# Optimization experiments

Measured on AMD Instinct MI355X. Metric: run time of the kernel, lower is better.

The kernel has to match this reference:

```python
import jax, jax.numpy as jnp
import numpy as np

B, V_IN, V_OUT, C_IN, C_OUT, K, NNZ = 16, 1024, 4096, 128, 256, 18, 16384

def setup_inputs() -> dict:
    key = jax.random.key(0)
    ks = jax.random.split(key, 10)
    def lin(k, fan_in, fan_out):
        s = 1.0 / np.sqrt(fan_in)
        return jax.random.normal(k, (fan_in, fan_out), jnp.float32) * s
    return {
        "x": jax.random.normal(ks[0], (B, V_IN, C_IN), jnp.float32),
        "vals": jax.random.uniform(ks[1], (NNZ,), jnp.float32),
        "W1": lin(ks[2], 1 * C_IN, C_OUT),
        "b1": jnp.zeros((C_OUT,), jnp.float32),
        "Wd3": lin(ks[3], (K // 3) * C_IN, C_OUT // 4),
        "bd3": jnp.zeros((C_OUT // 4,), jnp.float32),
        "W2d3": lin(ks[4], (K // 3 * 2) * C_IN, C_OUT // 4),
        "b2d3": jnp.zeros((C_OUT // 4,), jnp.float32),
        "Wf": lin(ks[5], K * C_IN, C_OUT // 2),
        "bf": jnp.zeros((C_OUT // 2,), jnp.float32),
        "rows": jax.random.randint(ks[6], (NNZ,), 0, V_OUT, jnp.int32),
        "cols": jax.random.randint(ks[7], (NNZ,), 0, V_IN, jnp.int32),
        "spiral_idx": jax.random.randint(ks[8], (V_OUT, K), 0, V_OUT, jnp.int32),
    }

def _pool(x, rows, cols, vals, dim_size):
    # sparse upsample: gather cols, scale, scatter-add to rows
    gathered = x[:, cols, :] * vals[None, :, None]  # [B, nnz, C]
    return jnp.zeros((x.shape[0], dim_size, x.shape[2]), x.dtype).at[:, rows, :].add(gathered)

def _spiral_conv(feat, idx, W, b):
    # gather fixed spiral neighborhoods then shared linear layer
    Bz, V, C = feat.shape[0], idx.shape[0], feat.shape[2]
    g = feat[:, idx.reshape(-1), :].reshape(Bz, V, idx.shape[1] * C)  # [B, V, K*C]
    return g @ W + b

def reference(x, vals, W1, b1, Wd3, bd3, W2d3, b2d3, Wf, bf, rows, cols, spiral_idx):
    out = _pool(x, rows, cols, vals, V_OUT)  # [B, V_OUT, C_IN]
    k = spiral_idx.shape[1]
    short_cut = _spiral_conv(out, spiral_idx[:, :1], W1, b1)
    p_d3 = _spiral_conv(out, spiral_idx[:, : k // 3], Wd3, bd3)
    p_2d3 = _spiral_conv(out, spiral_idx[:, : k // 3 * 2], W2d3, b2d3)
    p = _spiral_conv(out, spiral_idx, Wf, bf)
    f = jnp.concatenate((p, p_2d3, p_d3), axis=2)  # [B, V_OUT, C_OUT]
    return jax.nn.relu(short_cut + f)
```

## Files before the change

kernel.cpp:

```cpp
#include <hip/hip_runtime.h>
#include <hip/hip_bf16.h>

#define B_SZ   16
#define V_IN   1024
#define V_OUT  4096
#define C_IN   128
#define C_OUT  256
#define K_NB   18
#define NNZ    16384
#define K_GEMM (K_NB * C_IN)
#define BK     64
#define NKT    (K_GEMM / BK)

typedef __attribute__((ext_vector_type(8))) short bf16x8;
typedef __attribute__((ext_vector_type(4))) float f32x4;

#define GLOAD16(src, dst) __builtin_amdgcn_global_load_lds( \
    (const __attribute__((address_space(1))) unsigned int*)(src), \
    (__attribute__((address_space(3))) unsigned int*)(dst), 16, 0, 0)

__global__ void zero_counts_kernel(int* counts) {
    int i = blockIdx.x * blockDim.x + threadIdx.x;
    if (i < V_OUT) counts[i] = 0;
}

__global__ void hist_kernel(const int* __restrict__ rows, int* counts) {
    int n = blockIdx.x * blockDim.x + threadIdx.x;
    if (n < NNZ) atomicAdd(&counts[rows[n]], 1);
}

__global__ void scan_kernel(const int* __restrict__ counts, int* offsets, int* cursor) {
    __shared__ int s[1024];
    int t = threadIdx.x;
    int base = t * 4;
    int c0 = counts[base], c1 = counts[base + 1], c2 = counts[base + 2], c3 = counts[base + 3];
    int tot = c0 + c1 + c2 + c3;
    s[t] = tot;
    __syncthreads();
    for (int d = 1; d < 1024; d <<= 1) {
        int v = (t >= d) ? s[t - d] : 0;
        __syncthreads();
        s[t] += v;
        __syncthreads();
    }
    int excl = s[t] - tot;
    offsets[base]     = excl;
    offsets[base + 1] = excl + c0;
    offsets[base + 2] = excl + c0 + c1;
    offsets[base + 3] = excl + c0 + c1 + c2;
    cursor[base]     = excl;
    cursor[base + 1] = excl + c0;
    cursor[base + 2] = excl + c0 + c1;
    cursor[base + 3] = excl + c0 + c1 + c2;
    if (t == 1023) offsets[V_OUT] = s[1023];
}

__global__ void fill_kernel(const int* __restrict__ rows, int* cursor, int* perm) {
    int n = blockIdx.x * blockDim.x + threadIdx.x;
    if (n < NNZ) {
        int r = rows[n];
        int pos = atomicAdd(&cursor[r], 1);
        perm[pos] = n;
    }
}

__global__ __launch_bounds__(128) void pool_kernel(
    const float* __restrict__ x, const float* __restrict__ vals,
    const int* __restrict__ cols, const int* __restrict__ offsets,
    const int* __restrict__ perm, __hip_bfloat16* __restrict__ pool) {
    int r = blockIdx.x;
    int c = threadIdx.x;
    int j0 = offsets[r], j1 = offsets[r + 1];
    float acc[B_SZ];
#pragma unroll
    for (int b = 0; b < B_SZ; ++b) acc[b] = 0.f;
    for (int j = j0; j < j1; ++j) {
        int n = perm[j];
        float v = vals[n];
        const float* xp = x + (size_t)cols[n] * C_IN + c;
#pragma unroll
        for (int b = 0; b < B_SZ; ++b) acc[b] += v * xp[(size_t)b * V_IN * C_IN];
    }
#pragma unroll
    for (int b = 0; b < B_SZ; ++b)
        pool[((size_t)b * V_OUT + r) * C_IN + c] = __float2bfloat16(acc[b]);
}

__global__ void wcomb_kernel(const float* __restrict__ W1, const float* __restrict__ Wd3,
                             const float* __restrict__ W2d3, const float* __restrict__ Wf,
                             __hip_bfloat16* __restrict__ wTs) {
    int idx = blockIdx.x * blockDim.x + threadIdx.x;
    if (idx >= NKT * 16384) return;
    int kt = idx >> 14;
    int c  = (idx >> 3) & 2047;
    int e  = idx & 7;
    int nrow  = c >> 3;
    int kslot = (c & 7) << 4;
    int kb = kslot ^ ((nrow & 7) << 4);
    int r  = kt * 64 + (kb >> 1) + e;
    int col = nrow;
    float v;
    if (col < 128)      v = Wf[r * 128 + col];
    else if (col < 192) v = (r < 1536) ? W2d3[r * 64 + (col - 128)] : 0.f;
    else                v = (r < 768)  ? Wd3[r * 64 + (col - 192)]  : 0.f;
    if (r < 128) v += W1[r * 256 + col];
    wTs[idx] = __float2bfloat16(v);
}

__global__ void bias_kernel(const float* __restrict__ b1, const float* __restrict__ bd3,
                            const float* __restrict__ b2d3, const float* __restrict__ bf,
                            float* __restrict__ bias) {
    int c = threadIdx.x;
    float v = b1[c];
    if (c < 128)      v += bf[c];
    else if (c < 192) v += b2d3[c - 128];
    else              v += bd3[c - 192];
    bias[c] = v;
}

__global__ __launch_bounds__(512, 2) void gemm_kernel(
    const __hip_bfloat16* __restrict__ pool,
    const __hip_bfloat16* __restrict__ wTs,
    const float* __restrict__ bias,
    const int* __restrict__ spiral,
    float* __restrict__ out)
{
    __shared__ __align__(16) char smem[149504];
    int* spl = (int*)(smem + 131072);

    const int tid  = threadIdx.x;
    const int lane = tid & 63;
    const int wid  = tid >> 6;
    const int wm   = (wid >> 2) << 7;
    const int wn   = (wid & 3) << 6;

    const int bid = blockIdx.x;
    const int bm  = ((bid & 7) << 5) + (bid >> 3);
    const int b   = bm >> 4;
    const int v0  = (bm & 15) << 8;

    for (int i = tid; i < 256 * K_NB; i += 512) spl[i] = spiral[v0 * K_NB + i];
    __syncthreads();

    const char* poolBytes = (const char*)(pool + (size_t)b * V_OUT * C_IN);
    const char* wTsBytes  = (const char*)wTs;
    const int tg3 = tid >> 3;
    const int sb  = ((tid & 7) << 4) ^ ((tg3 & 7) << 4);

    auto stageA = [&](int kt) {
        const int j   = kt >> 1;
        const int c0b = (kt & 1) << 7;
        char* dst = smem + ((kt & 1) << 15);
#pragma unroll
        for (int ch = 0; ch < 4; ++ch) {
            int sidx = spl[(ch * 64 + tg3) * K_NB + j];
            GLOAD16(poolBytes + ((size_t)sidx << 8) + (c0b + sb),
                    dst + ((ch << 9) + tid) * 16);
        }
    };
    auto stageB = [&](int kt) {
        const char* src = wTsBytes + ((size_t)kt << 15) + tid * 16;
        char* dst = smem + 65536 + ((kt & 1) << 15);
#pragma unroll
        for (int ch = 0; ch < 4; ++ch)
            GLOAD16(src + (ch << 13), dst + (ch << 13) + tid * 16);
    };

    const int l15   = lane & 15;
    const int swm   = (lane & 7) << 4;
    const int klane = (lane >> 4) << 4;
    const int aRow  = (wm + l15) << 7;
    const int bRow  = (wn + l15) << 7;

    f32x4 acc[8][4] = {};

    stageA(0);
    stageB(0);

#pragma unroll 2
    for (int kt = 0; kt < NKT; ++kt) {
        const int s = kt & 1;
        const char* As = smem + (s << 15);
        const char* Bs = smem + 65536 + (s << 15);

        if (kt + 1 < NKT) {
            stageA(kt + 1);
            asm volatile("s_waitcnt vmcnt(4)" ::: "memory");
        } else {
            asm volatile("s_waitcnt vmcnt(0)" ::: "memory");
        }
        __builtin_amdgcn_s_barrier();
        __builtin_amdgcn_sched_barrier(0);

        bf16x8 a[8], b0, b1;
#pragma unroll
        for (int mi = 0; mi < 8; ++mi)
            a[mi] = *(const bf16x8*)(As + aRow + (mi << 11) + ((0 + klane) ^ swm));
        b0 = *(const bf16x8*)(Bs + bRow + (0 << 11) + ((0 + klane) ^ swm));
        b1 = *(const bf16x8*)(Bs + bRow + (1 << 11) + ((0 + klane) ^ swm));
        __builtin_amdgcn_s_setprio(1);
#pragma unroll
        for (int mi = 0; mi < 8; ++mi) {
            acc[mi][0] = __builtin_amdgcn_mfma_f32_16x16x32_bf16(a[mi], b0, acc[mi][0], 0, 0, 0);
            acc[mi][1] = __builtin_amdgcn_mfma_f32_16x16x32_bf16(a[mi], b1, acc[mi][1], 0, 0, 0);
        }
        __builtin_amdgcn_s_setprio(0);
        b0 = *(const bf16x8*)(Bs + bRow + (2 << 11) + ((0 + klane) ^ swm));
        b1 = *(const bf16x8*)(Bs + bRow + (3 << 11) + ((0 + klane) ^ swm));
        __builtin_amdgcn_s_setprio(1);
#pragma unroll
        for (int mi = 0; mi < 8; ++mi) {
            acc[mi][2] = __builtin_amdgcn_mfma_f32_16x16x32_bf16(a[mi], b0, acc[mi][2], 0, 0, 0);
            acc[mi][3] = __builtin_amdgcn_mfma_f32_16x16x32_bf16(a[mi], b1, acc[mi][3], 0, 0, 0);
        }
        __builtin_amdgcn_s_setprio(0);
        if (kt + 1 < NKT) stageB(kt + 1);
#pragma unroll
        for (int mi = 0; mi < 8; ++mi)
            a[mi] = *(const bf16x8*)(As + aRow + (mi << 11) + ((64 + klane) ^ swm));
        b0 = *(const bf16x8*)(Bs + bRow + (0 << 11) + ((64 + klane) ^ swm));
        b1 = *(const bf16x8*)(Bs + bRow + (1 << 11) + ((64 + klane) ^ swm));
        __builtin_amdgcn_s_setprio(1);
#pragma unroll
        for (int mi = 0; mi < 8; ++mi) {
            acc[mi][0] = __builtin_amdgcn_mfma_f32_16x16x32_bf16(a[mi], b0, acc[mi][0], 0, 0, 0);
            acc[mi][1] = __builtin_amdgcn_mfma_f32_16x16x32_bf16(a[mi], b1, acc[mi][1], 0, 0, 0);
        }
        __builtin_amdgcn_s_setprio(0);
        b0 = *(const bf16x8*)(Bs + bRow + (2 << 11) + ((64 + klane) ^ swm));
        b1 = *(const bf16x8*)(Bs + bRow + (3 << 11) + ((64 + klane) ^ swm));
        __builtin_amdgcn_s_setprio(1);
#pragma unroll
        for (int mi = 0; mi < 8; ++mi) {
            acc[mi][2] = __builtin_amdgcn_mfma_f32_16x16x32_bf16(a[mi], b0, acc[mi][2], 0, 0, 0);
            acc[mi][3] = __builtin_amdgcn_mfma_f32_16x16x32_bf16(a[mi], b1, acc[mi][3], 0, 0, 0);
        }
        __builtin_amdgcn_s_setprio(0);
        __builtin_amdgcn_s_barrier();
        __builtin_amdgcn_sched_barrier(0);
    }

#pragma unroll
    for (int ni = 0; ni < 4; ++ni) {
        int col = wn + ni * 16 + l15;
        float bz = bias[col];
#pragma unroll
        for (int mi = 0; mi < 8; ++mi) {
            int row0 = v0 + wm + mi * 16 + ((lane >> 4) << 2);
#pragma unroll
            for (int r4 = 0; r4 < 4; ++r4) {
                float v = acc[mi][ni][r4] + bz;
                out[((size_t)(b * V_OUT + row0 + r4)) * C_OUT + col] = v > 0.f ? v : 0.f;
            }
        }
    }
}

extern "C" void kernel_launch(void* const* d_in, const int* in_sizes, int n_in,
                              void* d_out, int out_size, void* d_ws, size_t ws_size,
                              hipStream_t stream) {
    const float* x     = (const float*)d_in[0];
    const float* vals  = (const float*)d_in[1];
    const float* W1    = (const float*)d_in[2];
    const float* b1    = (const float*)d_in[3];
    const float* Wd3   = (const float*)d_in[4];
    const float* bd3   = (const float*)d_in[5];
    const float* W2d3  = (const float*)d_in[6];
    const float* b2d3  = (const float*)d_in[7];
    const float* Wf    = (const float*)d_in[8];
    const float* bf    = (const float*)d_in[9];
    const int*   rows  = (const int*)d_in[10];
    const int*   cols  = (const int*)d_in[11];
    const int*   spiral= (const int*)d_in[12];
    float* out = (float*)d_out;

    char* ws = (char*)d_ws;
    __hip_bfloat16* pool = (__hip_bfloat16*)ws;
    __hip_bfloat16* wTs  = (__hip_bfloat16*)(ws + 16777216);
    float* bias          = (float*)(ws + 16777216 + 1179648);
    int*   counts        = (int*)(ws + 16777216 + 1179648 + 1024);
    int*   offsets       = counts + V_OUT;
    int*   cursor        = offsets + V_OUT + 4;
    int*   perm          = cursor + V_OUT;

    zero_counts_kernel<<<(V_OUT + 255) / 256, 256, 0, stream>>>(counts);
    hist_kernel<<<NNZ / 256, 256, 0, stream>>>(rows, counts);
    scan_kernel<<<1, 1024, 0, stream>>>(counts, offsets, cursor);
    fill_kernel<<<NNZ / 256, 256, 0, stream>>>(rows, cursor, perm);
    pool_kernel<<<V_OUT, C_IN, 0, stream>>>(x, vals, cols, offsets, perm, pool);
    wcomb_kernel<<<(NKT * 16384 + 255) / 256, 256, 0, stream>>>(W1, Wd3, W2d3, Wf, wTs);
    bias_kernel<<<1, C_OUT, 0, stream>>>(b1, bd3, b2d3, bf, bias);
    gemm_kernel<<<256, 512, 0, stream>>>(pool, wTs, bias, spiral, out);
}
```

Measured before the change: 112.0 us.

## Skip zero-weight K tiles per wave, fuse bias prep, faster scan

```diff
diff --git a/kernel.cpp b/kernel.cpp
--- a/kernel.cpp
+++ b/kernel.cpp
@@ -19,40 +19,40 @@
     (const __attribute__((address_space(1))) unsigned int*)(src), \
     (__attribute__((address_space(3))) unsigned int*)(dst), 16, 0, 0)
 
-__global__ void zero_counts_kernel(int* counts) {
-    int i = blockIdx.x * blockDim.x + threadIdx.x;
-    if (i < V_OUT) counts[i] = 0;
-}
-
 __global__ void hist_kernel(const int* __restrict__ rows, int* counts) {
     int n = blockIdx.x * blockDim.x + threadIdx.x;
     if (n < NNZ) atomicAdd(&counts[rows[n]], 1);
 }
 
 __global__ void scan_kernel(const int* __restrict__ counts, int* offsets, int* cursor) {
-    __shared__ int s[1024];
+    __shared__ int wsum[16];
     int t = threadIdx.x;
-    int base = t * 4;
-    int c0 = counts[base], c1 = counts[base + 1], c2 = counts[base + 2], c3 = counts[base + 3];
+    int lane = t & 63, wid = t >> 6;
+    int base4 = t * 4;
+    int c0 = counts[base4], c1 = counts[base4 + 1], c2 = counts[base4 + 2], c3 = counts[base4 + 3];
     int tot = c0 + c1 + c2 + c3;
-    s[t] = tot;
+    int v = tot;
+#pragma unroll
+    for (int d = 1; d < 64; d <<= 1) {
+        int u = __shfl_up(v, d);
+        if (lane >= d) v += u;
+    }
+    if (lane == 63) wsum[wid] = v;
     __syncthreads();
-    for (int d = 1; d < 1024; d <<= 1) {
-        int v = (t >= d) ? s[t - d] : 0;
-        __syncthreads();
-        s[t] += v;
-        __syncthreads();
-    }
-    int excl = s[t] - tot;
-    offsets[base]     = excl;
-    offsets[base + 1] = excl + c0;
-    offsets[base + 2] = excl + c0 + c1;
-    offsets[base + 3] = excl + c0 + c1 + c2;
-    cursor[base]     = excl;
-    cursor[base + 1] = excl + c0;
-    cursor[base + 2] = excl + c0 + c1;
-    cursor[base + 3] = excl + c0 + c1 + c2;
-    if (t == 1023) offsets[V_OUT] = s[1023];
+    int wbase = 0;
+#pragma unroll
+    for (int w = 0; w < 16; ++w) wbase += (w < wid) ? wsum[w] : 0;
+    int incl = wbase + v;
+    int excl = incl - tot;
+    offsets[base4]     = excl;
+    offsets[base4 + 1] = excl + c0;
+    offsets[base4 + 2] = excl + c0 + c1;
+    offsets[base4 + 3] = excl + c0 + c1 + c2;
+    cursor[base4]     = excl;
+    cursor[base4 + 1] = excl + c0;
+    cursor[base4 + 2] = excl + c0 + c1;
+    cursor[base4 + 3] = excl + c0 + c1 + c2;
+    if (t == 1023) offsets[V_OUT] = incl;
 }
 
 __global__ void fill_kernel(const int* __restrict__ rows, int* cursor, int* perm) {
@@ -88,9 +88,21 @@
 
 __global__ void wcomb_kernel(const float* __restrict__ W1, const float* __restrict__ Wd3,
                              const float* __restrict__ W2d3, const float* __restrict__ Wf,
-                             __hip_bfloat16* __restrict__ wTs) {
+                             const float* __restrict__ b1, const float* __restrict__ bd3,
+                             const float* __restrict__ b2d3, const float* __restrict__ bf,
+                             __hip_bfloat16* __restrict__ wTs, float* __restrict__ bias) {
     int idx = blockIdx.x * blockDim.x + threadIdx.x;
-    if (idx >= NKT * 16384) return;
+    if (idx >= NKT * 16384) {
+        int c = idx - NKT * 16384;
+        if (c < C_OUT) {
+            float v = b1[c];
+            if (c < 128)      v += bf[c];
+            else if (c < 192) v += b2d3[c - 128];
+            else              v += bd3[c - 192];
+            bias[c] = v;
+        }
+        return;
+    }
     int kt = idx >> 14;
     int c  = (idx >> 3) & 2047;
     int e  = idx & 7;
@@ -107,17 +119,6 @@
     wTs[idx] = __float2bfloat16(v);
 }
 
-__global__ void bias_kernel(const float* __restrict__ b1, const float* __restrict__ bd3,
-                            const float* __restrict__ b2d3, const float* __restrict__ bf,
-                            float* __restrict__ bias) {
-    int c = threadIdx.x;
-    float v = b1[c];
-    if (c < 128)      v += bf[c];
-    else if (c < 192) v += b2d3[c - 128];
-    else              v += bd3[c - 192];
-    bias[c] = v;
-}
-
 __global__ __launch_bounds__(512, 2) void gemm_kernel(
     const __hip_bfloat16* __restrict__ pool,
     const __hip_bfloat16* __restrict__ wTs,
@@ -133,6 +134,8 @@
     const int wid  = tid >> 6;
     const int wm   = (wid >> 2) << 7;
     const int wn   = (wid & 3) << 6;
+    const int q    = wid & 3;
+    const int myNKT = (q == 3) ? 12 : ((q == 2) ? 24 : NKT);
 
     const int bid = blockIdx.x;
     const int bm  = ((bid & 7) << 5) + (bid >> 3);
@@ -140,7 +143,8 @@
     const int v0  = (bm & 15) << 8;
 
     for (int i = tid; i < 256 * K_NB; i += 512) spl[i] = spiral[v0 * K_NB + i];
-    __syncthreads();
+    asm volatile("s_waitcnt vmcnt(0) lgkmcnt(0)" ::: "memory");
+    __builtin_amdgcn_s_barrier();
 
     const char* poolBytes = (const char*)(pool + (size_t)b * V_OUT * C_IN);
     const char* wTsBytes  = (const char*)wTs;
@@ -192,50 +196,59 @@
         __builtin_amdgcn_s_barrier();
         __builtin_amdgcn_sched_barrier(0);
 
-        bf16x8 a[8], b0, b1;
-#pragma unroll
-        for (int mi = 0; mi < 8; ++mi)
-            a[mi] = *(const bf16x8*)(As + aRow + (mi << 11) + ((0 + klane) ^ swm));
-        b0 = *(const bf16x8*)(Bs + bRow + (0 << 11) + ((0 + klane) ^ swm));
-        b1 = *(const bf16x8*)(Bs + bRow + (1 << 11) + ((0 + klane) ^ swm));
-        __builtin_amdgcn_s_setprio(1);
-#pragma unroll
-        for (int mi = 0; mi < 8; ++mi) {
-            acc[mi][0] = __builtin_amdgcn_mfma_f32_16x16x32_bf16(a[mi], b0, acc[mi][0], 0, 0, 0);
-            acc[mi][1] = __builtin_amdgcn_mfma_f32_16x16x32_bf16(a[mi], b1, acc[mi][1], 0, 0, 0);
-        }
-        __builtin_amdgcn_s_setprio(0);
-        b0 = *(const bf16x8*)(Bs + bRow + (2 << 11) + ((0 + klane) ^ swm));
-        b1 = *(const bf16x8*)(Bs + bRow + (3 << 11) + ((0 + klane) ^ swm));
-        __builtin_amdgcn_s_setprio(1);
-#pragma unroll
-        for (int mi = 0; mi < 8; ++mi) {
-            acc[mi][2] = __builtin_amdgcn_mfma_f32_16x16x32_bf16(a[mi], b0, acc[mi][2], 0, 0, 0);
-            acc[mi][3] = __builtin_amdgcn_mfma_f32_16x16x32_bf16(a[mi], b1, acc[mi][3], 0, 0, 0);
-        }
-        __builtin_amdgcn_s_setprio(0);
+        const bool act = kt < myNKT;
+        bf16x8 a[8], b0, b1, b2, b3;
+
+        if (act) {
+#pragma unroll
+            for (int mi = 0; mi < 8; ++mi)
+                a[mi] = *(const bf16x8*)(As + aRow + (mi << 11) + ((0 + klane) ^ swm));
+            b0 = *(const bf16x8*)(Bs + bRow + (0 << 11) + ((0 + klane) ^ swm));
+            b1 = *(const bf16x8*)(Bs + bRow + (1 << 11) + ((0 + klane) ^ swm));
+            __builtin_amdgcn_s_setprio(1);
+#pragma unroll
+            for (int mi = 0; mi < 8; ++mi) {
+                acc[mi][0] = __builtin_amdgcn_mfma_f32_16x16x32_bf16(a[mi], b0, acc[mi][0], 0, 0, 0);
+                acc[mi][1] = __builtin_amdgcn_mfma_f32_16x16x32_bf16(a[mi], b1, acc[mi][1], 0, 0, 0);
+            }
+            __builtin_amdgcn_s_setprio(0);
+            b2 = *(const bf16x8*)(Bs + bRow + (2 << 11) + ((0 + klane) ^ swm));
+            b3 = *(const bf16x8*)(Bs + bRow + (3 << 11) + ((0 + klane) ^ swm));
+            __builtin_amdgcn_s_setprio(1);
+#pragma unroll
+            for (int mi = 0; mi < 8; ++mi) {
+                acc[mi][2] = __builtin_amdgcn_mfma_f32_16x16x32_bf16(a[mi], b2, acc[mi][2], 0, 0, 0);
+                acc[mi][3] = __builtin_amdgcn_mfma_f32_16x16x32_bf16(a[mi], b3, acc[mi][3], 0, 0, 0);
+            }
+            __builtin_amdgcn_s_setprio(0);
+        }
+
         if (kt + 1 < NKT) stageB(kt + 1);
-#pragma unroll
-        for (int mi = 0; mi < 8; ++mi)
-            a[mi] = *(const bf16x8*)(As + aRow + (mi << 11) + ((64 + klane) ^ swm));
-        b0 = *(const bf16x8*)(Bs + bRow + (0 << 11) + ((64 + klane) ^ swm));
-        b1 = *(const bf16x8*)(Bs + bRow + (1 << 11) + ((64 + klane) ^ swm));
-        __builtin_amdgcn_s_setprio(1);
-#pragma unroll
-        for (int mi = 0; mi < 8; ++mi) {
-            acc[mi][0] = __builtin_amdgcn_mfma_f32_16x16x32_bf16(a[mi], b0, acc[mi][0], 0, 0, 0);
-            acc[mi][1] = __builtin_amdgcn_mfma_f32_16x16x32_bf16(a[mi], b1, acc[mi][1], 0, 0, 0);
-        }
-        __builtin_amdgcn_s_setprio(0);
-        b0 = *(const bf16x8*)(Bs + bRow + (2 << 11) + ((64 + klane) ^ swm));
-        b1 = *(const bf16x8*)(Bs + bRow + (3 << 11) + ((64 + klane) ^ swm));
-        __builtin_amdgcn_s_setprio(1);
-#pragma unroll
-        for (int mi = 0; mi < 8; ++mi) {
-            acc[mi][2] = __builtin_amdgcn_mfma_f32_16x16x32_bf16(a[mi], b0, acc[mi][2], 0, 0, 0);
-            acc[mi][3] = __builtin_amdgcn_mfma_f32_16x16x32_bf16(a[mi], b1, acc[mi][3], 0, 0, 0);
-        }
-        __builtin_amdgcn_s_setprio(0);
+
+        if (act) {
+#pragma unroll
+            for (int mi = 0; mi < 8; ++mi)
+                a[mi] = *(const bf16x8*)(As + aRow + (mi << 11) + ((64 + klane) ^ swm));
+            b0 = *(const bf16x8*)(Bs + bRow + (0 << 11) + ((64 + klane) ^ swm));
+            b1 = *(const bf16x8*)(Bs + bRow + (1 << 11) + ((64 + klane) ^ swm));
+            __builtin_amdgcn_s_setprio(1);
+#pragma unroll
+            for (int mi = 0; mi < 8; ++mi) {
+                acc[mi][0] = __builtin_amdgcn_mfma_f32_16x16x32_bf16(a[mi], b0, acc[mi][0], 0, 0, 0);
+                acc[mi][1] = __builtin_amdgcn_mfma_f32_16x16x32_bf16(a[mi], b1, acc[mi][1], 0, 0, 0);
+            }
+            __builtin_amdgcn_s_setprio(0);
+            b2 = *(const bf16x8*)(Bs + bRow + (2 << 11) + ((64 + klane) ^ swm));
+            b3 = *(const bf16x8*)(Bs + bRow + (3 << 11) + ((64 + klane) ^ swm));
+            __builtin_amdgcn_s_setprio(1);
+#pragma unroll
+            for (int mi = 0; mi < 8; ++mi) {
+                acc[mi][2] = __builtin_amdgcn_mfma_f32_16x16x32_bf16(a[mi], b2, acc[mi][2], 0, 0, 0);
+                acc[mi][3] = __builtin_amdgcn_mfma_f32_16x16x32_bf16(a[mi], b3, acc[mi][3], 0, 0, 0);
+            }
+            __builtin_amdgcn_s_setprio(0);
+        }
+
         __builtin_amdgcn_s_barrier();
         __builtin_amdgcn_sched_barrier(0);
     }
@@ -283,12 +296,12 @@
     int*   cursor        = offsets + V_OUT + 4;
     int*   perm          = cursor + V_OUT;
 
-    zero_counts_kernel<<<(V_OUT + 255) / 256, 256, 0, stream>>>(counts);
+    hipMemsetAsync(counts, 0, V_OUT * sizeof(int), stream);
     hist_kernel<<<NNZ / 256, 256, 0, stream>>>(rows, counts);
     scan_kernel<<<1, 1024, 0, stream>>>(counts, offsets, cursor);
     fill_kernel<<<NNZ / 256, 256, 0, stream>>>(rows, cursor, perm);
     pool_kernel<<<V_OUT, C_IN, 0, stream>>>(x, vals, cols, offsets, perm, pool);
-    wcomb_kernel<<<(NKT * 16384 + 255) / 256, 256, 0, stream>>>(W1, Wd3, W2d3, Wf, wTs);
-    bias_kernel<<<1, C_OUT, 0, stream>>>(b1, bd3, b2d3, bf, bias);
+    wcomb_kernel<<<(NKT * 16384 + C_OUT + 255) / 256, 256, 0, stream>>>(
+        W1, Wd3, W2d3, Wf, b1, bd3, b2d3, bf, wTs, bias);
     gemm_kernel<<<256, 512, 0, stream>>>(pool, wTs, bias, spiral, out);
 }
```

After: 108.8 us. 1.03x faster.
